# Performance work log

Hardware: AMD Instinct MI355X
Metric: run time of the kernel (lower is better)

The kernel has to match this reference:

```python
import jax, jax.numpy as jnp
import numpy as np

N_NODES = 100000
N_EDGES = 3200000
D_IN = 256
D_OUT = 256


def setup_inputs() -> dict:
    key = jax.random.key(0)
    k1, k2, k3, k4, k5 = jax.random.split(key, 5)
    X = jax.random.normal(k1, (N_NODES, D_IN), dtype=jnp.float32)
    A_rows = jax.random.randint(k2, (N_EDGES,), 0, N_NODES, dtype=jnp.int64)
    A_cols = jax.random.randint(k3, (N_EDGES,), 0, N_NODES, dtype=jnp.int64)
    A_vals = jax.random.uniform(k4, (N_EDGES,), dtype=jnp.float32)
    # Xavier-uniform init of nn.Linear(in_dim, out_dim, bias=False): W is [out, in]
    limit = float(np.sqrt(6.0 / (D_IN + D_OUT)))
    W = jax.random.uniform(k5, (D_OUT, D_IN), minval=-limit, maxval=limit,
                           dtype=jnp.float32)
    return {"X": X, "A_rows": A_rows, "A_cols": A_cols, "A_vals": A_vals, "W": W}


def reference(X, A_rows, A_cols, A_vals, W):
    # AX = A_coo @ X : gather source features, scale by edge value, scatter-add by row
    msgs = X[A_cols] * A_vals[:, None]                  # [E, D_in]
    AX = jax.ops.segment_sum(msgs, A_rows, num_segments=N_NODES)  # [N, D_in]
    # Linear (bias=False) then ReLU; dropout p=0.0 is identity
    H = jax.nn.relu(AX @ W.T)                           # [N, D_out]
    return H
```

## Files before the change

kernel.cpp:

```cpp
#include <hip/hip_runtime.h>
#include <hip/hip_bf16.h>

#define N_NODES 100000
#define N_EDGES 3200000
#define D 256
#define SHIFT 9
#define NB 196
#define EPB 4096

typedef __attribute__((ext_vector_type(8))) short short8;
typedef __attribute__((ext_vector_type(4))) float f32x4;

__device__ inline short bfbits(float x) {
    __hip_bfloat16 h = __float2bfloat16(x);
    return __builtin_bit_cast(short, h);
}

__device__ inline short8 load_cvt8(const float* __restrict__ p) {
    float4 a = *(const float4*)p;
    float4 b = *(const float4*)(p + 4);
    short8 r;
    r[0] = bfbits(a.x); r[1] = bfbits(a.y); r[2] = bfbits(a.z); r[3] = bfbits(a.w);
    r[4] = bfbits(b.x); r[5] = bfbits(b.y); r[6] = bfbits(b.z); r[7] = bfbits(b.w);
    return r;
}

__device__ inline int block_excl_scan_256(int c, int* wsum, int& total) {
    const int lane = threadIdx.x & 63, wid = threadIdx.x >> 6;
    int v = c;
    #pragma unroll
    for (int off = 1; off < 64; off <<= 1) {
        int u = __shfl_up(v, off);
        if (lane >= off) v += u;
    }
    if (lane == 63) wsum[wid] = v;
    __syncthreads();
    int w0 = wsum[0], w1 = wsum[1], w2 = wsum[2], w3 = wsum[3];
    total = w0 + w1 + w2 + w3;
    int wex = (wid > 0 ? w0 : 0) + (wid > 1 ? w1 : 0) + (wid > 2 ? w2 : 0);
    return wex + v - c;
}

__global__ __launch_bounds__(256) void bucket_hist(
    const int* __restrict__ rows, int* __restrict__ gcnt, int nE)
{
    __shared__ int h[NB];
    for (int i = threadIdx.x; i < NB; i += 256) h[i] = 0;
    __syncthreads();
    for (int e = blockIdx.x * 256 + threadIdx.x; e < nE; e += gridDim.x * 256)
        atomicAdd(&h[rows[e] >> SHIFT], 1);
    __syncthreads();
    for (int i = threadIdx.x; i < NB; i += 256)
        if (h[i]) atomicAdd(&gcnt[i], h[i]);
}

__global__ __launch_bounds__(256) void bucket_scan(
    const int* __restrict__ gcnt, int* __restrict__ bbase,
    int* __restrict__ gcursor, int* __restrict__ row_ptr)
{
    __shared__ int wsum[4];
    int c = (threadIdx.x < NB) ? gcnt[threadIdx.x] : 0;
    int total;
    int ex = block_excl_scan_256(c, wsum, total);
    if (threadIdx.x < NB) { bbase[threadIdx.x] = ex; gcursor[threadIdx.x] = ex; }
    if (threadIdx.x == 0) { bbase[NB] = total; row_ptr[N_NODES] = total; }
}

__global__ __launch_bounds__(256) void bucket_split(
    const int* __restrict__ rows, const int* __restrict__ cols,
    const float* __restrict__ vals, int* __restrict__ gcursor,
    int2* __restrict__ bcv, int nE)
{
    __shared__ int cnt[256];
    __shared__ int startp[256];
    __shared__ int posp[256];
    __shared__ int gb[256];
    __shared__ int wsum[4];
    __shared__ int2 scv[EPB];
    const int t  = threadIdx.x;
    const int e0 = blockIdx.x * EPB;

    cnt[t] = 0;
    __syncthreads();

    int   myrow[16];
    int   mycol[16];
    float myval[16];
    #pragma unroll
    for (int k = 0; k < 16; ++k) {
        int e = e0 + k * 256 + t;
        if (e < nE) {
            myrow[k] = rows[e]; mycol[k] = cols[e]; myval[k] = vals[e];
            atomicAdd(&cnt[myrow[k] >> SHIFT], 1);
        } else {
            myrow[k] = -1; mycol[k] = 0; myval[k] = 0.f;
        }
    }
    __syncthreads();

    int c = cnt[t];
    int total;
    int ex = block_excl_scan_256(c, wsum, total);
    startp[t] = ex;
    posp[t]   = ex;
    if (t < NB && c) gb[t] = atomicAdd(&gcursor[t], c);
    __syncthreads();

    #pragma unroll
    for (int k = 0; k < 16; ++k) {
        if (myrow[k] >= 0) {
            int b = myrow[k] >> SHIFT;
            int p = atomicAdd(&posp[b], 1);
            scv[p] = make_int2(((myrow[k] & 511) << 17) | mycol[k],
                               __float_as_int(myval[k]));
        }
    }
    __syncthreads();

    const int lane = t & 63, wid = t >> 6;
    for (int b = wid; b < NB; b += 4) {
        int cb = cnt[b];
        if (!cb) continue;
        int st = startp[b], g = gb[b];
        for (int i = lane; i < cb; i += 64)
            bcv[g + i] = scv[st + i];
    }
}

__global__ __launch_bounds__(256) void bucket_to_csr(
    const int* __restrict__ bbase, const int2* __restrict__ bcv,
    int* __restrict__ row_ptr, int2* __restrict__ cedge)
{
    __shared__ int hist[512];
    __shared__ int cur[512];
    __shared__ int wsum[4];
    const int t  = threadIdx.x;
    const int b  = blockIdx.x;
    const int r0 = b << SHIFT;
    const int s  = bbase[b], e = bbase[b + 1];

    hist[t] = 0; hist[t + 256] = 0;
    __syncthreads();
    for (int j = s + t; j < e; j += 256)
        atomicAdd(&hist[(unsigned)bcv[j].x >> 17], 1);
    __syncthreads();

    int c0 = hist[2 * t], c1 = hist[2 * t + 1];
    int total;
    int ex = block_excl_scan_256(c0 + c1, wsum, total);
    cur[2 * t]     = s + ex;
    cur[2 * t + 1] = s + ex + c0;
    int r = r0 + 2 * t;
    if (r     < N_NODES) row_ptr[r]     = s + ex;
    if (r + 1 < N_NODES) row_ptr[r + 1] = s + ex + c0;
    __syncthreads();

    for (int j = s + t; j < e; j += 256) {
        int2 q = bcv[j];
        int rl = (unsigned)q.x >> 17;
        int p = atomicAdd(&cur[rl], 1);
        cedge[p] = make_int2(q.x & 0x1FFFF, q.y);
    }
}

__global__ __launch_bounds__(256) void gemm_bf16(
    const float* __restrict__ X,
    const float* __restrict__ W,
    unsigned short* __restrict__ Y,
    int M)
{
    const int wid  = threadIdx.x >> 6;
    const int lane = threadIdx.x & 63;
    const int m0   = blockIdx.x * 64;
    const int n0   = wid * 64;
    const int lr   = lane & 15;
    const int ko   = (lane >> 4) * 8;

    f32x4 acc[4][4] = {};

    #pragma unroll
    for (int k0 = 0; k0 < 256; k0 += 32) {
        short8 bfrag[4], afrag[4];
        #pragma unroll
        for (int j = 0; j < 4; ++j)
            bfrag[j] = load_cvt8(W + (size_t)(n0 + j * 16 + lr) * 256 + k0 + ko);
        #pragma unroll
        for (int i = 0; i < 4; ++i) {
            int r = m0 + i * 16 + lr;
            if (r > M - 1) r = M - 1;
            afrag[i] = load_cvt8(X + (size_t)r * 256 + k0 + ko);
        }
        #pragma unroll
        for (int i = 0; i < 4; ++i)
            #pragma unroll
            for (int j = 0; j < 4; ++j)
                acc[i][j] = __builtin_amdgcn_mfma_f32_16x16x32_bf16(
                    afrag[i], bfrag[j], acc[i][j], 0, 0, 0);
    }

    #pragma unroll
    for (int i = 0; i < 4; ++i) {
        int rbase = m0 + i * 16 + (lane >> 4) * 4;
        #pragma unroll
        for (int rr = 0; rr < 4; ++rr) {
            int r = rbase + rr;
            if (r < M) {
                #pragma unroll
                for (int j = 0; j < 4; ++j)
                    Y[(size_t)r * 256 + n0 + j * 16 + lr] =
                        (unsigned short)bfbits(acc[i][j][rr]);
            }
        }
    }
}

__global__ __launch_bounds__(256) void spmm_gather_relu(
    const unsigned short* __restrict__ Y,
    const int* __restrict__ row_ptr,
    const int2* __restrict__ cedge,
    float* __restrict__ H)
{
    int row  = blockIdx.x * 4 + (threadIdx.x >> 6);
    int lane = threadIdx.x & 63;
    if (row >= N_NODES) return;
    int s = row_ptr[row];
    int e = row_ptr[row + 1];

    float4 acc = make_float4(0.f, 0.f, 0.f, 0.f);
    const int fo = lane * 4;

    for (int base = s; base < e; base += 64) {
        int idx = base + lane;
        int2 q = make_int2(0, 0);
        if (idx < e) q = cedge[idx];
        int cnt = min(64, e - base);
        int j = 0;
        for (; j + 4 <= cnt; j += 4) {
            int c0 = __builtin_amdgcn_readfirstlane(__shfl(q.x, j));
            int c1 = __builtin_amdgcn_readfirstlane(__shfl(q.x, j + 1));
            int c2 = __builtin_amdgcn_readfirstlane(__shfl(q.x, j + 2));
            int c3 = __builtin_amdgcn_readfirstlane(__shfl(q.x, j + 3));
            float v0 = __int_as_float(__builtin_amdgcn_readfirstlane(__shfl(q.y, j)));
            float v1 = __int_as_float(__builtin_amdgcn_readfirstlane(__shfl(q.y, j + 1)));
            float v2 = __int_as_float(__builtin_amdgcn_readfirstlane(__shfl(q.y, j + 2)));
            float v3 = __int_as_float(__builtin_amdgcn_readfirstlane(__shfl(q.y, j + 3)));
            ushort4 y0 = *(const ushort4*)(Y + (size_t)c0 * 256 + fo);
            ushort4 y1 = *(const ushort4*)(Y + (size_t)c1 * 256 + fo);
            ushort4 y2 = *(const ushort4*)(Y + (size_t)c2 * 256 + fo);
            ushort4 y3 = *(const ushort4*)(Y + (size_t)c3 * 256 + fo);
            acc.x += __uint_as_float((unsigned)y0.x << 16) * v0;
            acc.y += __uint_as_float((unsigned)y0.y << 16) * v0;
            acc.z += __uint_as_float((unsigned)y0.z << 16) * v0;
            acc.w += __uint_as_float((unsigned)y0.w << 16) * v0;
            acc.x += __uint_as_float((unsigned)y1.x << 16) * v1;
            acc.y += __uint_as_float((unsigned)y1.y << 16) * v1;
            acc.z += __uint_as_float((unsigned)y1.z << 16) * v1;
            acc.w += __uint_as_float((unsigned)y1.w << 16) * v1;
            acc.x += __uint_as_float((unsigned)y2.x << 16) * v2;
            acc.y += __uint_as_float((unsigned)y2.y << 16) * v2;
            acc.z += __uint_as_float((unsigned)y2.z << 16) * v2;
            acc.w += __uint_as_float((unsigned)y2.w << 16) * v2;
            acc.x += __uint_as_float((unsigned)y3.x << 16) * v3;
            acc.y += __uint_as_float((unsigned)y3.y << 16) * v3;
            acc.z += __uint_as_float((unsigned)y3.z << 16) * v3;
            acc.w += __uint_as_float((unsigned)y3.w << 16) * v3;
        }
        for (; j < cnt; ++j) {
            int   cj = __builtin_amdgcn_readfirstlane(__shfl(q.x, j));
            float vj = __int_as_float(__builtin_amdgcn_readfirstlane(__shfl(q.y, j)));
            ushort4 y4 = *(const ushort4*)(Y + (size_t)cj * 256 + fo);
            acc.x += __uint_as_float((unsigned)y4.x << 16) * vj;
            acc.y += __uint_as_float((unsigned)y4.y << 16) * vj;
            acc.z += __uint_as_float((unsigned)y4.z << 16) * vj;
            acc.w += __uint_as_float((unsigned)y4.w << 16) * vj;
        }
    }
    float4 r;
    r.x = acc.x > 0.f ? acc.x : 0.f;
    r.y = acc.y > 0.f ? acc.y : 0.f;
    r.z = acc.z > 0.f ? acc.z : 0.f;
    r.w = acc.w > 0.f ? acc.w : 0.f;
    ((float4*)(H + (size_t)row * 256))[lane] = r;
}


extern "C" void kernel_launch(void* const* d_in, const int* in_sizes, int n_in,
                              void* d_out, int out_size, void* d_ws, size_t ws_size,
                              hipStream_t stream) {
    const float* X    = (const float*)d_in[0];
    const int*   rows = (const int*)d_in[1];
    const int*   cols = (const int*)d_in[2];
    const float* vals = (const float*)d_in[3];
    const float* W    = (const float*)d_in[4];
    float*       H    = (float*)d_out;

    char* ws = (char*)d_ws;
    unsigned short* Y       = (unsigned short*)(ws);
    int*            row_ptr = (int*)(ws + 51200000);
    int2*           cedge   = (int2*)(ws + 51600896);
    int2*           bcv     = (int2*)(ws + 77200896);
    int*            gcnt    = (int*)(ws + 102800896);
    int*            bbase   = (int*)(ws + 102801920);
    int*            gcursor = (int*)(ws + 102802944);

    hipMemsetAsync(gcnt, 0, NB * sizeof(int), stream);

    bucket_hist<<<256, 256, 0, stream>>>(rows, gcnt, N_EDGES);
    bucket_scan<<<1, 256, 0, stream>>>(gcnt, bbase, gcursor, row_ptr);
    bucket_split<<<(N_EDGES + EPB - 1) / EPB, 256, 0, stream>>>(
        rows, cols, vals, gcursor, bcv, N_EDGES);
    bucket_to_csr<<<NB, 256, 0, stream>>>(bbase, bcv, row_ptr, cedge);

    gemm_bf16<<<(N_NODES + 63) / 64, 256, 0, stream>>>(X, W, Y, N_NODES);

    spmm_gather_relu<<<(N_NODES + 3) / 4, 256, 0, stream>>>(Y, row_ptr, cedge, H);
}
```

Measured before the change: 451.2 us.

## Fuse bucket split and GEMM into one launch; simplify split scatter

Merges the bucket_split and gemm_bf16 kernels into a single launch in which the first blocks do the edge bucketing and the rest do the bf16 MFMA GEMM, so the two independent stages can run concurrently and one launch is dropped. The split path also stops staging edges in LDS and scanning per block: it reserves global slots per bucket and writes each edge straight to its slot with shared atomics. That removes the LDS staging and the coalesced copy-out, but the bcv writes become scattered and uncoalesced, and GEMM blocks now share the register and LDS budget of the fused kernel.

```diff
diff --git a/kernel.cpp b/kernel.cpp
--- a/kernel.cpp
+++ b/kernel.cpp
@@ -7,6 +7,8 @@
 #define SHIFT 9
 #define NB 196
 #define EPB 4096
+#define NSPLIT 782
+#define NGEMM 1563
 
 typedef __attribute__((ext_vector_type(8))) short short8;
 typedef __attribute__((ext_vector_type(4))) float f32x4;
@@ -66,64 +68,96 @@
     if (threadIdx.x == 0) { bbase[NB] = total; row_ptr[N_NODES] = total; }
 }
 
-__global__ __launch_bounds__(256) void bucket_split(
+__global__ __launch_bounds__(256) void split_gemm(
     const int* __restrict__ rows, const int* __restrict__ cols,
     const float* __restrict__ vals, int* __restrict__ gcursor,
-    int2* __restrict__ bcv, int nE)
-{
-    __shared__ int cnt[256];
-    __shared__ int startp[256];
-    __shared__ int posp[256];
-    __shared__ int gb[256];
-    __shared__ int wsum[4];
-    __shared__ int2 scv[EPB];
-    const int t  = threadIdx.x;
-    const int e0 = blockIdx.x * EPB;
-
-    cnt[t] = 0;
-    __syncthreads();
-
-    int   myrow[16];
-    int   mycol[16];
-    float myval[16];
-    #pragma unroll
-    for (int k = 0; k < 16; ++k) {
-        int e = e0 + k * 256 + t;
-        if (e < nE) {
-            myrow[k] = rows[e]; mycol[k] = cols[e]; myval[k] = vals[e];
-            atomicAdd(&cnt[myrow[k] >> SHIFT], 1);
-        } else {
-            myrow[k] = -1; mycol[k] = 0; myval[k] = 0.f;
-        }
-    }
-    __syncthreads();
-
-    int c = cnt[t];
-    int total;
-    int ex = block_excl_scan_256(c, wsum, total);
-    startp[t] = ex;
-    posp[t]   = ex;
-    if (t < NB && c) gb[t] = atomicAdd(&gcursor[t], c);
-    __syncthreads();
-
-    #pragma unroll
-    for (int k = 0; k < 16; ++k) {
-        if (myrow[k] >= 0) {
-            int b = myrow[k] >> SHIFT;
-            int p = atomicAdd(&posp[b], 1);
-            scv[p] = make_int2(((myrow[k] & 511) << 17) | mycol[k],
-                               __float_as_int(myval[k]));
-        }
-    }
-    __syncthreads();
-
-    const int lane = t & 63, wid = t >> 6;
-    for (int b = wid; b < NB; b += 4) {
-        int cb = cnt[b];
-        if (!cb) continue;
-        int st = startp[b], g = gb[b];
-        for (int i = lane; i < cb; i += 64)
-            bcv[g + i] = scv[st + i];
+    int2* __restrict__ bcv,
+    const float* __restrict__ X, const float* __restrict__ W,
+    unsigned short* __restrict__ Y, int nE)
+{
+    if (blockIdx.x < NSPLIT) {
+        __shared__ int cnt[256];
+        __shared__ int posp[256];
+        const int t  = threadIdx.x;
+        const int e0 = blockIdx.x * EPB;
+
+        cnt[t] = 0;
+        __syncthreads();
+
+        int  myb[16];
+        int2 mycv[16];
+        #pragma unroll
+        for (int k = 0; k < 16; ++k) {
+            int e = e0 + k * 256 + t;
+            if (e < nE) {
+                int r = rows[e];
+                myb[k]  = r >> SHIFT;
+                mycv[k] = make_int2(((r & 511) << 17) | cols[e],
+                                    __float_as_int(vals[e]));
+                atomicAdd(&cnt[myb[k]], 1);
+            } else {
+                myb[k] = -1;
+            }
+        }
+        __syncthreads();
+        if (t < NB) {
+            int c = cnt[t];
+            posp[t] = c ? atomicAdd(&gcursor[t], c) : 0;
+        }
+        __syncthreads();
+        #pragma unroll
+        for (int k = 0; k < 16; ++k) {
+            if (myb[k] >= 0) {
+                int p = atomicAdd(&posp[myb[k]], 1);
+                bcv[p] = mycv[k];
+            }
+        }
+    } else {
+        const int bid  = blockIdx.x - NSPLIT;
+        const int wid  = threadIdx.x >> 6;
+        const int lane = threadIdx.x & 63;
+        const int m0   = bid * 64;
+        const int n0   = wid * 64;
+        const int lr   = lane & 15;
+        const int ko   = (lane >> 4) * 8;
+        const int M    = N_NODES;
+
+        f32x4 acc[4][4] = {};
+
+        #pragma unroll
+        for (int k0 = 0; k0 < 256; k0 += 32) {
+            short8 bfrag[4], afrag[4];
+            #pragma unroll
+            for (int j = 0; j < 4; ++j)
+                bfrag[j] = load_cvt8(W + (size_t)(n0 + j * 16 + lr) * 256 + k0 + ko);
+            #pragma unroll
+            for (int i = 0; i < 4; ++i) {
+                int r = m0 + i * 16 + lr;
+                if (r > M - 1) r = M - 1;
+                afrag[i] = load_cvt8(X + (size_t)r * 256 + k0 + ko);
+            }
+            #pragma unroll
+            for (int i = 0; i < 4; ++i)
+                #pragma unroll
+                for (int j = 0; j < 4; ++j)
+                    acc[i][j] = __builtin_amdgcn_mfma_f32_16x16x32_bf16(
+                        afrag[i], bfrag[j], acc[i][j], 0, 0, 0);
+        }
+
+        #pragma unroll
+        for (int i = 0; i < 4; ++i) {
+            int rbase = m0 + i * 16 + (lane >> 4) * 4;
+            #pragma unroll
+            for (int rr = 0; rr < 4; ++rr) {
+                int r = rbase + rr;
+                if (r < M) {
+                    #pragma unroll
+                    for (int j = 0; j < 4; ++j)
+                        Y[(size_t)r * 256 + n0 + j * 16 + lr] =
+                            (unsigned short)bfbits(acc[i][j][rr]);
+                }
+            }
+        }
     }
 }
 
@@ -160,57 +194,6 @@
         int rl = (unsigned)q.x >> 17;
         int p = atomicAdd(&cur[rl], 1);
         cedge[p] = make_int2(q.x & 0x1FFFF, q.y);
-    }
-}
-
-__global__ __launch_bounds__(256) void gemm_bf16(
-    const float* __restrict__ X,
-    const float* __restrict__ W,
-    unsigned short* __restrict__ Y,
-    int M)
-{
-    const int wid  = threadIdx.x >> 6;
-    const int lane = threadIdx.x & 63;
-    const int m0   = blockIdx.x * 64;
-    const int n0   = wid * 64;
-    const int lr   = lane & 15;
-    const int ko   = (lane >> 4) * 8;
-
-    f32x4 acc[4][4] = {};
-
-    #pragma unroll
-    for (int k0 = 0; k0 < 256; k0 += 32) {
-        short8 bfrag[4], afrag[4];
-        #pragma unroll
-        for (int j = 0; j < 4; ++j)
-            bfrag[j] = load_cvt8(W + (size_t)(n0 + j * 16 + lr) * 256 + k0 + ko);
-        #pragma unroll
-        for (int i = 0; i < 4; ++i) {
-            int r = m0 + i * 16 + lr;
-            if (r > M - 1) r = M - 1;
-            afrag[i] = load_cvt8(X + (size_t)r * 256 + k0 + ko);
-        }
-        #pragma unroll
-        for (int i = 0; i < 4; ++i)
-            #pragma unroll
-            for (int j = 0; j < 4; ++j)
-                acc[i][j] = __builtin_amdgcn_mfma_f32_16x16x32_bf16(
-                    afrag[i], bfrag[j], acc[i][j], 0, 0, 0);
-    }
-
-    #pragma unroll
-    for (int i = 0; i < 4; ++i) {
-        int rbase = m0 + i * 16 + (lane >> 4) * 4;
-        #pragma unroll
-        for (int rr = 0; rr < 4; ++rr) {
-            int r = rbase + rr;
-            if (r < M) {
-                #pragma unroll
-                for (int j = 0; j < 4; ++j)
-                    Y[(size_t)r * 256 + n0 + j * 16 + lr] =
-                        (unsigned short)bfbits(acc[i][j][rr]);
-            }
-        }
     }
 }
 
@@ -307,11 +290,9 @@
 
     bucket_hist<<<256, 256, 0, stream>>>(rows, gcnt, N_EDGES);
     bucket_scan<<<1, 256, 0, stream>>>(gcnt, bbase, gcursor, row_ptr);
-    bucket_split<<<(N_EDGES + EPB - 1) / EPB, 256, 0, stream>>>(
-        rows, cols, vals, gcursor, bcv, N_EDGES);
+    split_gemm<<<NSPLIT + NGEMM, 256, 0, stream>>>(
+        rows, cols, vals, gcursor, bcv, X, W, Y, N_EDGES);
     bucket_to_csr<<<NB, 256, 0, stream>>>(bbase, bcv, row_ptr, cedge);
 
-    gemm_bf16<<<(N_NODES + 63) / 64, 256, 0, stream>>>(X, W, Y, N_NODES);
-
     spmm_gather_relu<<<(N_NODES + 3) / 4, 256, 0, stream>>>(Y, row_ptr, cedge, H);
 }
```

Measured after the change: 456.9 us. Within noise of the previous version (+1.3%).
